# Kernel tuning notes

Hardware: AMD Instinct MI355X
Metric: run time of the kernel (lower is better)

The kernel has to match this reference:

```python
import jax, jax.numpy as jnp
import numpy as np

N, F, H, G = 8192, 128, 64, 4      # nodes, node_attr_size, hidden_size, num groups
CONV_TH = 1e-05
MAX_ITER = 5


def setup_inputs() -> dict:
    key = jax.random.key(0)
    k1, k2, k3, k4 = jax.random.split(key, 4)
    X = jax.random.normal(k1, (N, F), dtype=jnp.float32)
    # L scaled like a normalized graph operator so the fixed-point is well-behaved
    L = jax.random.normal(k2, (N, N), dtype=jnp.float32) * (1.0 / np.sqrt(N))
    # reservoir weights (requires_grad=False in the original, still materialized here)
    W_ih = jax.random.normal(k3, (G, H, F), dtype=jnp.float32) * (1.0 / np.sqrt(F))
    W_hh = jax.random.normal(k4, (G, H, H), dtype=jnp.float32) * (0.9 / np.sqrt(H))
    return {"X": X, "L": L, "W_ih": W_ih, "W_hh": W_hh}


def _gesn_forward(X, L, W_ih, W_hh):
    # wiu = linear(X, W_ih) per group: [G, N, H]
    wiu = jnp.einsum('nf,ghf->gnh', X, W_ih)
    hx0 = jnp.zeros((G, N, H), dtype=X.dtype)
    done0 = jnp.zeros((G,), dtype=bool)

    def step(carry, _):
        hx, done = carry
        lin = jnp.einsum('gnh,gkh->gnk', hx, W_hh)          # linear(hx, W_hh)
        new = jnp.tanh(wiu + jnp.einsum('nm,gmk->gnk', L, lin))  # mm(L, .) + wiu, tanh activation
        diff = jnp.sqrt(jnp.sum((new - hx) ** 2, axis=(1, 2)))   # ||last_res - res|| per group
        hx_next = jnp.where(done[:, None, None], hx, new)   # masked early-exit (mimics break)
        done = done | (diff < CONV_TH)
        return (hx_next, done), None

    (hx, _), _ = jax.lax.scan(step, (hx0, done0), None, length=MAX_ITER)
    # concat group outputs along feature dim -> [N, G*H]
    return jnp.transpose(hx, (1, 0, 2)).reshape(N, G * H)


def reference(X, L, W_ih, W_hh):
    return _gesn_forward(X, L, W_ih, W_hh)
```

## Files before the change

### kernel.cpp

```cpp
#include <hip/hip_runtime.h>
#include <hip/hip_fp16.h>

#define NN 8192
#define FF 128
#define HH 64
#define GG 4
#define CONV_TH2 1e-10f

typedef _Float16 half8 __attribute__((ext_vector_type(8)));
typedef float floatx4 __attribute__((ext_vector_type(4)));

#define OFF_WIU  134217728ull
#define OFF_LIN  142606336ull
#define OFF_CP   146800640ull
#define OFF_META 180355072ull

__device__ __forceinline__ void load16(const void* g, void* l) {
  __builtin_amdgcn_global_load_lds((const __attribute__((address_space(1))) void*)g,
                                   (__attribute__((address_space(3))) void*)l,
                                   16, 0, 0);
}

#define BAR()  __builtin_amdgcn_s_barrier()
#define WAITV(N) asm volatile("s_waitcnt vmcnt(" #N ")" ::: "memory")
#define WAITL()  asm volatile("s_waitcnt lgkmcnt(0)" ::: "memory")

__global__ __launch_bounds__(256) void k_convert(const float* __restrict__ L,
                                                 _Float16* __restrict__ Lh,
                                                 float* __restrict__ diffsq) {
  if (blockIdx.x == 0 && threadIdx.x < 32) diffsq[threadIdx.x] = 0.f;
  size_t i = ((size_t)blockIdx.x * 256 + threadIdx.x) * 8;
  float4 a = *(const float4*)(L + i);
  float4 b = *(const float4*)(L + i + 4);
  half8 h;
  h[0] = (_Float16)a.x; h[1] = (_Float16)a.y; h[2] = (_Float16)a.z; h[3] = (_Float16)a.w;
  h[4] = (_Float16)b.x; h[5] = (_Float16)b.y; h[6] = (_Float16)b.z; h[7] = (_Float16)b.w;
  *(half8*)(Lh + i) = h;
}

__global__ __launch_bounds__(256) void k_wiu(const float* __restrict__ X,
    const float* __restrict__ Wih, const float* __restrict__ Whh,
    float* __restrict__ wiu, float* __restrict__ hx,
    _Float16* __restrict__ lin_t, float* __restrict__ diffsq) {
  __shared__ __align__(16) float smem[2 * 64 * 128];
  float* Xs = smem;
  float* Ws = smem + 64 * 128;
  const int bx = blockIdx.x, g = blockIdx.y;
  const int t = threadIdx.x;
  const int m0 = bx * 64;
  #pragma unroll
  for (int p = 0; p < 8; ++p) {
    int idx = p * 256 + t;
    int row = idx >> 5;
    int c4 = idx & 31;
    int sw = (c4 ^ (row >> 2)) & 31;
    float4 xv = *(const float4*)(X + (size_t)(m0 + row) * FF + c4 * 4);
    *(float4*)(Xs + row * 128 + sw * 4) = xv;
    float4 wv = *(const float4*)(Wih + (size_t)g * HH * FF + (size_t)row * FF + c4 * 4);
    *(float4*)(Ws + row * 128 + sw * 4) = wv;
  }
  __syncthreads();
  const int tc = t & 15, tm = t >> 4;
  float acc[4][4];
  #pragma unroll
  for (int r = 0; r < 4; ++r)
    #pragma unroll
    for (int s = 0; s < 4; ++s) acc[r][s] = 0.f;
  for (int f4 = 0; f4 < 32; ++f4) {
    float4 xv[4], wv[4];
    #pragma unroll
    for (int r = 0; r < 4; ++r) {
      int m = tm * 4 + r;
      xv[r] = *(const float4*)(Xs + m * 128 + (((f4 ^ (m >> 2)) & 31) * 4));
    }
    #pragma unroll
    for (int s = 0; s < 4; ++s) {
      int c = tc * 4 + s;
      wv[s] = *(const float4*)(Ws + c * 128 + (((f4 ^ (c >> 2)) & 31) * 4));
    }
    #pragma unroll
    for (int r = 0; r < 4; ++r)
      #pragma unroll
      for (int s = 0; s < 4; ++s)
        acc[r][s] += xv[r].x * wv[s].x + xv[r].y * wv[s].y +
                     xv[r].z * wv[s].z + xv[r].w * wv[s].w;
  }
  __syncthreads();
  float* hxs = smem;
  float* Whs = smem + 64 * 65;
  float diffp = 0.f;
  #pragma unroll
  for (int r = 0; r < 4; ++r) {
    int ml = tm * 4 + r;
    size_t off = (size_t)(m0 + ml) * 256 + g * 64 + tc * 4;
    float4 wv = make_float4(acc[r][0], acc[r][1], acc[r][2], acc[r][3]);
    *(float4*)(wiu + off) = wv;
    float4 hv;
    hv.x = tanhf(wv.x); hv.y = tanhf(wv.y); hv.z = tanhf(wv.z); hv.w = tanhf(wv.w);
    *(float4*)(hx + off) = hv;
    hxs[ml * 65 + tc * 4 + 0] = hv.x;
    hxs[ml * 65 + tc * 4 + 1] = hv.y;
    hxs[ml * 65 + tc * 4 + 2] = hv.z;
    hxs[ml * 65 + tc * 4 + 3] = hv.w;
    diffp += hv.x * hv.x + hv.y * hv.y + hv.z * hv.z + hv.w * hv.w;
  }
  #pragma unroll
  for (int p = 0; p < 16; ++p) {
    int idx = p * 256 + t;
    Whs[(idx >> 6) * 65 + (idx & 63)] = Whh[(size_t)g * HH * HH + idx];
  }
  for (int o = 32; o; o >>= 1) diffp += __shfl_down(diffp, o);
  if ((t & 63) == 0) atomicAdd(diffsq + g, diffp);
  __syncthreads();
  const int ml = t & 63, wv_ = t >> 6;
  float lacc[16];
  #pragma unroll
  for (int i = 0; i < 16; ++i) lacc[i] = 0.f;
  for (int h = 0; h < 64; ++h) {
    float xh = hxs[ml * 65 + h];
    #pragma unroll
    for (int i = 0; i < 16; ++i)
      lacc[i] += xh * Whs[(wv_ + 4 * i) * 65 + h];
  }
  #pragma unroll
  for (int i = 0; i < 16; ++i)
    lin_t[(size_t)(g * 64 + wv_ + 4 * i) * NN + m0 + ml] = (_Float16)lacc[i];
}


__device__ __forceinline__ void g_stage(const _Float16* ga, const _Float16* gb,
                                        _Float16* da, _Float16* db) {
  load16(ga,            da);
  load16(ga + 64 * NN,  da + 4096);
  load16(gb,            db);
  load16(gb + 64 * NN,  db + 4096);
  load16(gb + 128 * NN, db + 8192);
  load16(gb + 192 * NN, db + 12288);
}

__device__ __forceinline__ void g_compute(const _Float16* sb,
    const int (&aoffs)[2][4], const int (&boffs)[2][4], floatx4 (&acc)[4][4]) {
  #pragma unroll
  for (int ks = 0; ks < 2; ++ks) {
    half8 af[4], bf[4];
    #pragma unroll
    for (int mt = 0; mt < 4; ++mt) af[mt] = *(const half8*)(sb + aoffs[ks][mt]);
    #pragma unroll
    for (int nt = 0; nt < 4; ++nt) bf[nt] = *(const half8*)(sb + 8192 + boffs[ks][nt]);
    #pragma unroll
    for (int mt = 0; mt < 4; ++mt)
      #pragma unroll
      for (int nt = 0; nt < 4; ++nt)
        acc[mt][nt] = __builtin_amdgcn_mfma_f32_16x16x32_f16(af[mt], bf[nt], acc[mt][nt], 0, 0, 0);
  }
}

__global__ __launch_bounds__(512, 2) void k_gemm(const _Float16* __restrict__ A,
    const _Float16* __restrict__ Bt, float* __restrict__ Cp) {
  __shared__ __align__(16) _Float16 smem[3 * 24576];
  const int bx = blockIdx.x;
  const int bz = blockIdx.y;
  const int t = threadIdx.x;
  const int lane = t & 63, wid = t >> 6;
  const int wr = wid >> 2, wc = wid & 3;
  const int l15 = lane & 15, quad = lane >> 4;
  const size_t m0 = (size_t)bx * 128;
  const size_t k0 = (size_t)bz * 2048;

  const int r_ = t >> 3;
  const int j_ = (t & 7) ^ (r_ & 7);
  const _Float16* ga = A  + (m0 + r_) * NN + k0 + (size_t)j_ * 8;
  const _Float16* gb = Bt + (size_t)r_ * NN + k0 + (size_t)j_ * 8;
  _Float16* dA0 = smem + t * 8;                 _Float16* dB0 = dA0 + 8192;
  _Float16* dA1 = smem + 24576 + t * 8;         _Float16* dB1 = dA1 + 8192;
  _Float16* dA2 = smem + 49152 + t * 8;         _Float16* dB2 = dA2 + 8192;
  const _Float16* sb0 = smem;
  const _Float16* sb1 = smem + 24576;
  const _Float16* sb2 = smem + 49152;

  int aoffs[2][4], boffs[2][4];
  #pragma unroll
  for (int ks = 0; ks < 2; ++ks) {
    #pragma unroll
    for (int mt = 0; mt < 4; ++mt) {
      int m = wr * 64 + mt * 16 + l15;
      aoffs[ks][mt] = m * 64 + (((ks * 4 + quad) ^ (m & 7)) * 8);
    }
    #pragma unroll
    for (int nt = 0; nt < 4; ++nt) {
      int n = wc * 64 + nt * 16 + l15;
      boffs[ks][nt] = n * 64 + (((ks * 4 + quad) ^ (n & 7)) * 8);
    }
  }
  floatx4 acc[4][4];
  #pragma unroll
  for (int mt = 0; mt < 4; ++mt)
    #pragma unroll
    for (int nt = 0; nt < 4; ++nt)
      acc[mt][nt] = (floatx4){0.f, 0.f, 0.f, 0.f};

  g_stage(ga, gb, dA0, dB0); ga += 64; gb += 64;
  g_stage(ga, gb, dA1, dB1); ga += 64; gb += 64;
  #pragma unroll 1
  for (int grp = 0; grp < 10; ++grp) {
    g_stage(ga, gb, dA2, dB2); ga += 64; gb += 64;
    WAITV(12); BAR();
    g_compute(sb0, aoffs, boffs, acc);
    WAITL(); BAR();
    g_stage(ga, gb, dA0, dB0); ga += 64; gb += 64;
    WAITV(12); BAR();
    g_compute(sb1, aoffs, boffs, acc);
    WAITL(); BAR();
    g_stage(ga, gb, dA1, dB1); ga += 64; gb += 64;
    WAITV(12); BAR();
    g_compute(sb2, aoffs, boffs, acc);
    WAITL(); BAR();
  }
  WAITV(6); BAR();
  g_compute(sb0, aoffs, boffs, acc);
  WAITV(0); BAR();
  g_compute(sb1, aoffs, boffs, acc);

  float* Cb = Cp + (size_t)bz * NN * 256;
  #pragma unroll
  for (int mt = 0; mt < 4; ++mt) {
    #pragma unroll
    for (int nt = 0; nt < 4; ++nt) {
      size_t gm = m0 + wr * 64 + mt * 16 + quad * 4;
      size_t gc = (size_t)wc * 64 + nt * 16 + l15;
      #pragma unroll
      for (int rg = 0; rg < 4; ++rg)
        Cb[(gm + rg) * 256 + gc] = acc[mt][nt][rg];
    }
  }
}

__global__ __launch_bounds__(256) void k_post(const float* __restrict__ Cp,
    const float* __restrict__ wiu, const float* __restrict__ Whh,
    float* __restrict__ hx, _Float16* __restrict__ lin_t,
    float* __restrict__ diffsq, int it, int write_lin) {
  __shared__ float hxs[64 * 65];
  __shared__ float Whs[64 * 65];
  const int bx = blockIdx.x, g = blockIdx.y, t = threadIdx.x;
  const int m0 = bx * 64;
  const int tcol = t & 15, trow = t >> 4;
  int dn = 0;
  #pragma unroll
  for (int j = 0; j < 4; ++j)
    if (j < it) dn |= (diffsq[j * GG + g] < CONV_TH2) ? 1 : 0;
  float diffp = 0.f;
  #pragma unroll
  for (int p = 0; p < 4; ++p) {
    int ml = p * 16 + trow;
    size_t off = (size_t)(m0 + ml) * 256 + g * 64 + tcol * 4;
    float4 s  = *(const float4*)(Cp + off);
    float4 q1 = *(const float4*)(Cp + (size_t)1 * NN * 256 + off);
    float4 q2 = *(const float4*)(Cp + (size_t)2 * NN * 256 + off);
    float4 q3 = *(const float4*)(Cp + (size_t)3 * NN * 256 + off);
    s.x += q1.x + q2.x + q3.x; s.y += q1.y + q2.y + q3.y;
    s.z += q1.z + q2.z + q3.z; s.w += q1.w + q2.w + q3.w;
    float4 wv = *(const float4*)(wiu + off);
    float4 old = *(const float4*)(hx + off);
    float4 nv;
    nv.x = tanhf(wv.x + s.x); nv.y = tanhf(wv.y + s.y);
    nv.z = tanhf(wv.z + s.z); nv.w = tanhf(wv.w + s.w);
    float4 ov;
    ov.x = dn ? old.x : nv.x; ov.y = dn ? old.y : nv.y;
    ov.z = dn ? old.z : nv.z; ov.w = dn ? old.w : nv.w;
    *(float4*)(hx + off) = ov;
    float dx = nv.x - old.x, dy = nv.y - old.y, dz = nv.z - old.z, dw = nv.w - old.w;
    diffp += dx * dx + dy * dy + dz * dz + dw * dw;
    hxs[ml * 65 + tcol * 4 + 0] = ov.x;
    hxs[ml * 65 + tcol * 4 + 1] = ov.y;
    hxs[ml * 65 + tcol * 4 + 2] = ov.z;
    hxs[ml * 65 + tcol * 4 + 3] = ov.w;
  }
  if (write_lin) {
    #pragma unroll
    for (int p = 0; p < 16; ++p) {
      int idx = p * 256 + t;
      Whs[(idx >> 6) * 65 + (idx & 63)] = Whh[(size_t)g * HH * HH + idx];
    }
  }
  for (int o = 32; o; o >>= 1) diffp += __shfl_down(diffp, o);
  if ((t & 63) == 0) atomicAdd(diffsq + it * GG + g, diffp);
  if (!write_lin) return;
  __syncthreads();
  const int ml = t & 63, wv_ = t >> 6;
  float lacc[16];
  #pragma unroll
  for (int i = 0; i < 16; ++i) lacc[i] = 0.f;
  for (int h = 0; h < 64; ++h) {
    float xh = hxs[ml * 65 + h];
    #pragma unroll
    for (int i = 0; i < 16; ++i)
      lacc[i] += xh * Whs[(wv_ + 4 * i) * 65 + h];
  }
  #pragma unroll
  for (int i = 0; i < 16; ++i)
    lin_t[(size_t)(g * 64 + wv_ + 4 * i) * NN + m0 + ml] = (_Float16)lacc[i];
}

extern "C" void kernel_launch(void* const* d_in, const int* in_sizes, int n_in,
                              void* d_out, int out_size, void* d_ws, size_t ws_size,
                              hipStream_t stream) {
  const float* X   = (const float*)d_in[0];
  const float* L   = (const float*)d_in[1];
  const float* Wih = (const float*)d_in[2];
  const float* Whh = (const float*)d_in[3];
  float* out = (float*)d_out;
  char* ws = (char*)d_ws;
  _Float16* Lh    = (_Float16*)ws;
  float*    wiu   = (float*)(ws + OFF_WIU);
  _Float16* lin_t = (_Float16*)(ws + OFF_LIN);
  float*    Cp    = (float*)(ws + OFF_CP);
  float*    diffsq = (float*)(ws + OFF_META);

  k_convert<<<32768, 256, 0, stream>>>(L, Lh, diffsq);
  k_wiu<<<dim3(128, 4), 256, 0, stream>>>(X, Wih, Whh, wiu, out, lin_t, diffsq);
  for (int it = 1; it <= 4; ++it) {
    k_gemm<<<dim3(64, 4), 512, 0, stream>>>(Lh, lin_t, Cp);
    k_post<<<dim3(128, 4), 256, 0, stream>>>(Cp, wiu, Whh, out, lin_t, diffsq,
                                             it, (it < 4) ? 1 : 0);
  }
}
```

Measured before the change: 721.7 us.

## Fuse GEMM and post iterations into one persistent cooperative kernel

Replaces the four pairs of k_gemm/k_post launches with a single cooperative kernel of 256 blocks. It loops over iterations and uses grid.sync between the split-K GEMM phase and the tanh/convergence/lin phase. The post phase now runs on the same blocks with a 128-row by group tiling, and MFMA compute sections raise wave priority with s_setprio. This removes the per-launch overhead and gaps between launches. In exchange it adds grid-wide barrier costs and reuses GEMM shared memory for the post phase.

```diff
diff --git a/kernel.cpp b/kernel.cpp
--- a/kernel.cpp
+++ b/kernel.cpp
@@ -1,5 +1,8 @@
 #include <hip/hip_runtime.h>
 #include <hip/hip_fp16.h>
+#include <hip/hip_cooperative_groups.h>
+
+namespace cg = cooperative_groups;
 
 #define NN 8192
 #define FF 128
@@ -140,6 +143,7 @@
 
 __device__ __forceinline__ void g_compute(const _Float16* sb,
     const int (&aoffs)[2][4], const int (&boffs)[2][4], floatx4 (&acc)[4][4]) {
+  __builtin_amdgcn_s_setprio(1);
   #pragma unroll
   for (int ks = 0; ks < 2; ++ks) {
     half8 af[4], bf[4];
@@ -153,31 +157,33 @@
       for (int nt = 0; nt < 4; ++nt)
         acc[mt][nt] = __builtin_amdgcn_mfma_f32_16x16x32_f16(af[mt], bf[nt], acc[mt][nt], 0, 0, 0);
   }
-}
-
-__global__ __launch_bounds__(512, 2) void k_gemm(const _Float16* __restrict__ A,
-    const _Float16* __restrict__ Bt, float* __restrict__ Cp) {
+  __builtin_amdgcn_s_setprio(0);
+}
+
+__global__ __launch_bounds__(512, 2) void k_iter(
+    const _Float16* __restrict__ A, const float* __restrict__ wiu,
+    const float* __restrict__ Whh, float* __restrict__ hx,
+    _Float16* __restrict__ lin_t, float* __restrict__ Cp,
+    float* __restrict__ diffsq) {
   __shared__ __align__(16) _Float16 smem[3 * 24576];
-  const int bx = blockIdx.x;
-  const int bz = blockIdx.y;
+  cg::grid_group grid = cg::this_grid();
+  const int bid = blockIdx.x;
   const int t = threadIdx.x;
+
   const int lane = t & 63, wid = t >> 6;
   const int wr = wid >> 2, wc = wid & 3;
   const int l15 = lane & 15, quad = lane >> 4;
-  const size_t m0 = (size_t)bx * 128;
+  const int bx = bid >> 2, bz = bid & 3;
+  const size_t m0g = (size_t)bx * 128;
   const size_t k0 = (size_t)bz * 2048;
-
   const int r_ = t >> 3;
   const int j_ = (t & 7) ^ (r_ & 7);
-  const _Float16* ga = A  + (m0 + r_) * NN + k0 + (size_t)j_ * 8;
-  const _Float16* gb = Bt + (size_t)r_ * NN + k0 + (size_t)j_ * 8;
   _Float16* dA0 = smem + t * 8;                 _Float16* dB0 = dA0 + 8192;
   _Float16* dA1 = smem + 24576 + t * 8;         _Float16* dB1 = dA1 + 8192;
   _Float16* dA2 = smem + 49152 + t * 8;         _Float16* dB2 = dA2 + 8192;
   const _Float16* sb0 = smem;
   const _Float16* sb1 = smem + 24576;
   const _Float16* sb2 = smem + 49152;
-
   int aoffs[2][4], boffs[2][4];
   #pragma unroll
   for (int ks = 0; ks < 2; ++ks) {
@@ -192,113 +198,113 @@
       boffs[ks][nt] = n * 64 + (((ks * 4 + quad) ^ (n & 7)) * 8);
     }
   }
-  floatx4 acc[4][4];
-  #pragma unroll
-  for (int mt = 0; mt < 4; ++mt)
-    #pragma unroll
-    for (int nt = 0; nt < 4; ++nt)
-      acc[mt][nt] = (floatx4){0.f, 0.f, 0.f, 0.f};
-
-  g_stage(ga, gb, dA0, dB0); ga += 64; gb += 64;
-  g_stage(ga, gb, dA1, dB1); ga += 64; gb += 64;
-  #pragma unroll 1
-  for (int grp = 0; grp < 10; ++grp) {
-    g_stage(ga, gb, dA2, dB2); ga += 64; gb += 64;
-    WAITV(12); BAR();
+  const int pg = bid & 3, prb = bid >> 2;
+  const int m0p = prb * 128;
+  const int tcol = t & 15, trow = t >> 4;
+  float* hxs = (float*)smem;
+  float* Whs = hxs + 128 * 65;
+
+  for (int it = 1; it <= 4; ++it) {
+    const _Float16* ga = A     + (m0g + r_) * NN + k0 + (size_t)j_ * 8;
+    const _Float16* gb = lin_t + (size_t)r_ * NN + k0 + (size_t)j_ * 8;
+    floatx4 acc[4][4];
+    #pragma unroll
+    for (int mt = 0; mt < 4; ++mt)
+      #pragma unroll
+      for (int nt = 0; nt < 4; ++nt)
+        acc[mt][nt] = (floatx4){0.f, 0.f, 0.f, 0.f};
+    g_stage(ga, gb, dA0, dB0); ga += 64; gb += 64;
+    g_stage(ga, gb, dA1, dB1); ga += 64; gb += 64;
+    #pragma unroll 1
+    for (int grp = 0; grp < 10; ++grp) {
+      g_stage(ga, gb, dA2, dB2); ga += 64; gb += 64;
+      WAITV(12); BAR();
+      g_compute(sb0, aoffs, boffs, acc);
+      WAITL(); BAR();
+      g_stage(ga, gb, dA0, dB0); ga += 64; gb += 64;
+      WAITV(12); BAR();
+      g_compute(sb1, aoffs, boffs, acc);
+      WAITL(); BAR();
+      g_stage(ga, gb, dA1, dB1); ga += 64; gb += 64;
+      WAITV(12); BAR();
+      g_compute(sb2, aoffs, boffs, acc);
+      WAITL(); BAR();
+    }
+    WAITV(6); BAR();
     g_compute(sb0, aoffs, boffs, acc);
-    WAITL(); BAR();
-    g_stage(ga, gb, dA0, dB0); ga += 64; gb += 64;
-    WAITV(12); BAR();
+    WAITV(0); BAR();
     g_compute(sb1, aoffs, boffs, acc);
-    WAITL(); BAR();
-    g_stage(ga, gb, dA1, dB1); ga += 64; gb += 64;
-    WAITV(12); BAR();
-    g_compute(sb2, aoffs, boffs, acc);
-    WAITL(); BAR();
-  }
-  WAITV(6); BAR();
-  g_compute(sb0, aoffs, boffs, acc);
-  WAITV(0); BAR();
-  g_compute(sb1, aoffs, boffs, acc);
-
-  float* Cb = Cp + (size_t)bz * NN * 256;
-  #pragma unroll
-  for (int mt = 0; mt < 4; ++mt) {
-    #pragma unroll
-    for (int nt = 0; nt < 4; ++nt) {
-      size_t gm = m0 + wr * 64 + mt * 16 + quad * 4;
-      size_t gc = (size_t)wc * 64 + nt * 16 + l15;
-      #pragma unroll
-      for (int rg = 0; rg < 4; ++rg)
-        Cb[(gm + rg) * 256 + gc] = acc[mt][nt][rg];
-    }
-  }
-}
-
-__global__ __launch_bounds__(256) void k_post(const float* __restrict__ Cp,
-    const float* __restrict__ wiu, const float* __restrict__ Whh,
-    float* __restrict__ hx, _Float16* __restrict__ lin_t,
-    float* __restrict__ diffsq, int it, int write_lin) {
-  __shared__ float hxs[64 * 65];
-  __shared__ float Whs[64 * 65];
-  const int bx = blockIdx.x, g = blockIdx.y, t = threadIdx.x;
-  const int m0 = bx * 64;
-  const int tcol = t & 15, trow = t >> 4;
-  int dn = 0;
-  #pragma unroll
-  for (int j = 0; j < 4; ++j)
-    if (j < it) dn |= (diffsq[j * GG + g] < CONV_TH2) ? 1 : 0;
-  float diffp = 0.f;
-  #pragma unroll
-  for (int p = 0; p < 4; ++p) {
-    int ml = p * 16 + trow;
-    size_t off = (size_t)(m0 + ml) * 256 + g * 64 + tcol * 4;
-    float4 s  = *(const float4*)(Cp + off);
-    float4 q1 = *(const float4*)(Cp + (size_t)1 * NN * 256 + off);
-    float4 q2 = *(const float4*)(Cp + (size_t)2 * NN * 256 + off);
-    float4 q3 = *(const float4*)(Cp + (size_t)3 * NN * 256 + off);
-    s.x += q1.x + q2.x + q3.x; s.y += q1.y + q2.y + q3.y;
-    s.z += q1.z + q2.z + q3.z; s.w += q1.w + q2.w + q3.w;
-    float4 wv = *(const float4*)(wiu + off);
-    float4 old = *(const float4*)(hx + off);
-    float4 nv;
-    nv.x = tanhf(wv.x + s.x); nv.y = tanhf(wv.y + s.y);
-    nv.z = tanhf(wv.z + s.z); nv.w = tanhf(wv.w + s.w);
-    float4 ov;
-    ov.x = dn ? old.x : nv.x; ov.y = dn ? old.y : nv.y;
-    ov.z = dn ? old.z : nv.z; ov.w = dn ? old.w : nv.w;
-    *(float4*)(hx + off) = ov;
-    float dx = nv.x - old.x, dy = nv.y - old.y, dz = nv.z - old.z, dw = nv.w - old.w;
-    diffp += dx * dx + dy * dy + dz * dz + dw * dw;
-    hxs[ml * 65 + tcol * 4 + 0] = ov.x;
-    hxs[ml * 65 + tcol * 4 + 1] = ov.y;
-    hxs[ml * 65 + tcol * 4 + 2] = ov.z;
-    hxs[ml * 65 + tcol * 4 + 3] = ov.w;
-  }
-  if (write_lin) {
-    #pragma unroll
-    for (int p = 0; p < 16; ++p) {
-      int idx = p * 256 + t;
-      Whs[(idx >> 6) * 65 + (idx & 63)] = Whh[(size_t)g * HH * HH + idx];
-    }
-  }
-  for (int o = 32; o; o >>= 1) diffp += __shfl_down(diffp, o);
-  if ((t & 63) == 0) atomicAdd(diffsq + it * GG + g, diffp);
-  if (!write_lin) return;
-  __syncthreads();
-  const int ml = t & 63, wv_ = t >> 6;
-  float lacc[16];
-  #pragma unroll
-  for (int i = 0; i < 16; ++i) lacc[i] = 0.f;
-  for (int h = 0; h < 64; ++h) {
-    float xh = hxs[ml * 65 + h];
-    #pragma unroll
-    for (int i = 0; i < 16; ++i)
-      lacc[i] += xh * Whs[(wv_ + 4 * i) * 65 + h];
-  }
-  #pragma unroll
-  for (int i = 0; i < 16; ++i)
-    lin_t[(size_t)(g * 64 + wv_ + 4 * i) * NN + m0 + ml] = (_Float16)lacc[i];
+    float* Cb = Cp + (size_t)bz * NN * 256;
+    #pragma unroll
+    for (int mt = 0; mt < 4; ++mt) {
+      #pragma unroll
+      for (int nt = 0; nt < 4; ++nt) {
+        size_t gm = m0g + wr * 64 + mt * 16 + quad * 4;
+        size_t gc = (size_t)wc * 64 + nt * 16 + l15;
+        #pragma unroll
+        for (int rg = 0; rg < 4; ++rg)
+          Cb[(gm + rg) * 256 + gc] = acc[mt][nt][rg];
+      }
+    }
+    grid.sync();
+    int dn = 0;
+    #pragma unroll
+    for (int j = 0; j < 4; ++j)
+      if (j < it) dn |= (diffsq[j * GG + pg] < CONV_TH2) ? 1 : 0;
+    float diffp = 0.f;
+    #pragma unroll
+    for (int p = 0; p < 4; ++p) {
+      int ml = p * 32 + trow;
+      size_t off = (size_t)(m0p + ml) * 256 + pg * 64 + tcol * 4;
+      float4 s  = *(const float4*)(Cp + off);
+      float4 q1 = *(const float4*)(Cp + (size_t)1 * NN * 256 + off);
+      float4 q2 = *(const float4*)(Cp + (size_t)2 * NN * 256 + off);
+      float4 q3 = *(const float4*)(Cp + (size_t)3 * NN * 256 + off);
+      s.x += q1.x + q2.x + q3.x; s.y += q1.y + q2.y + q3.y;
+      s.z += q1.z + q2.z + q3.z; s.w += q1.w + q2.w + q3.w;
+      float4 wv = *(const float4*)(wiu + off);
+      float4 old = *(const float4*)(hx + off);
+      float4 nv;
+      nv.x = tanhf(wv.x + s.x); nv.y = tanhf(wv.y + s.y);
+      nv.z = tanhf(wv.z + s.z); nv.w = tanhf(wv.w + s.w);
+      float4 ov;
+      ov.x = dn ? old.x : nv.x; ov.y = dn ? old.y : nv.y;
+      ov.z = dn ? old.z : nv.z; ov.w = dn ? old.w : nv.w;
+      *(float4*)(hx + off) = ov;
+      float dx = nv.x - old.x, dy = nv.y - old.y, dz = nv.z - old.z, dw = nv.w - old.w;
+      diffp += dx * dx + dy * dy + dz * dz + dw * dw;
+      hxs[ml * 65 + tcol * 4 + 0] = ov.x;
+      hxs[ml * 65 + tcol * 4 + 1] = ov.y;
+      hxs[ml * 65 + tcol * 4 + 2] = ov.z;
+      hxs[ml * 65 + tcol * 4 + 3] = ov.w;
+    }
+    if (it < 4) {
+      #pragma unroll
+      for (int p = 0; p < 8; ++p) {
+        int idx = p * 512 + t;
+        Whs[(idx >> 6) * 65 + (idx & 63)] = Whh[(size_t)pg * HH * HH + idx];
+      }
+    }
+    for (int o = 32; o; o >>= 1) diffp += __shfl_down(diffp, o);
+    if ((t & 63) == 0) atomicAdd(diffsq + it * GG + pg, diffp);
+    if (it < 4) {
+      __syncthreads();
+      const int ml2 = t & 127, wv2 = t >> 7;
+      float lacc[16];
+      #pragma unroll
+      for (int i = 0; i < 16; ++i) lacc[i] = 0.f;
+      for (int h = 0; h < 64; ++h) {
+        float xh = hxs[ml2 * 65 + h];
+        #pragma unroll
+        for (int i = 0; i < 16; ++i)
+          lacc[i] += xh * Whs[(wv2 + 4 * i) * 65 + h];
+      }
+      #pragma unroll
+      for (int i = 0; i < 16; ++i)
+        lin_t[(size_t)(pg * 64 + wv2 + 4 * i) * NN + m0p + ml2] = (_Float16)lacc[i];
+      grid.sync();
+    }
+  }
 }
 
 extern "C" void kernel_launch(void* const* d_in, const int* in_sizes, int n_in,
@@ -318,9 +324,16 @@
 
   k_convert<<<32768, 256, 0, stream>>>(L, Lh, diffsq);
   k_wiu<<<dim3(128, 4), 256, 0, stream>>>(X, Wih, Whh, wiu, out, lin_t, diffsq);
-  for (int it = 1; it <= 4; ++it) {
-    k_gemm<<<dim3(64, 4), 512, 0, stream>>>(Lh, lin_t, Cp);
-    k_post<<<dim3(128, 4), 256, 0, stream>>>(Cp, wiu, Whh, out, lin_t, diffsq,
-                                             it, (it < 4) ? 1 : 0);
-  }
-}
+
+  const _Float16* A_p = Lh;
+  const float* wiu_p = wiu;
+  const float* Whh_p = Whh;
+  float* hx_p = out;
+  _Float16* lin_p = lin_t;
+  float* Cp_p = Cp;
+  float* diffsq_p = diffsq;
+  void* args[7] = {(void*)&A_p, (void*)&wiu_p, (void*)&Whh_p, (void*)&hx_p,
+                   (void*)&lin_p, (void*)&Cp_p, (void*)&diffsq_p};
+  hipLaunchCooperativeKernel((const void*)k_iter, dim3(256), dim3(512),
+                             args, 0, stream);
+}
```

Result: slower. 961.2 us (+33.2%).
